# Performance work log

Hardware: AMD Instinct MI355X
Metric: run time of the kernel (lower is better)

The kernel has to match this reference:

```python
import jax, jax.numpy as jnp
import numpy as np

CH = 256
DQK = CH // 8

def setup_inputs() -> dict:
    key = jax.random.key(0)
    ks = jax.random.split(key, 8)
    x = jax.random.normal(ks[0], (4, 64, 64, CH), dtype=jnp.float32)
    # 1x1 convs == per-position linear layers: weight [Cin, Cout], bias [Cout]
    Wq = jax.random.normal(ks[1], (CH, DQK), dtype=jnp.float32) * 0.05
    bq = jnp.zeros((DQK,), dtype=jnp.float32)
    Wk = jax.random.normal(ks[2], (CH, DQK), dtype=jnp.float32) * 0.05
    bk = jnp.zeros((DQK,), dtype=jnp.float32)
    Wv = jax.random.normal(ks[3], (CH, CH), dtype=jnp.float32) * 0.05
    bv = jnp.zeros((CH,), dtype=jnp.float32)
    gamma = jnp.asarray(0.5, dtype=jnp.float32)  # nonzero so attention path matters
    return {"x": x, "Wq": Wq, "bq": bq, "Wk": Wk, "bk": bk, "Wv": Wv, "bv": bv, "gamma": gamma}

def reference(x, Wq, bq, Wk, bk, Wv, bv, gamma):
    B, H, W, C = x.shape
    N = H * W
    xf = x.reshape(B, N, C)                      # flatten spatial positions
    q = xf @ Wq + bq                             # [B, N, C/8]
    k = xf @ Wk + bk                             # [B, N, C/8]
    v = xf @ Wv + bv                             # [B, N, C]
    # Note: original applies NO 1/sqrt(d) scaling
    scores = jnp.einsum('bnd,bmd->bnm', q, k)    # [B, N, N]
    attn = jax.nn.softmax(scores, axis=-1)
    out = jnp.einsum('bnm,bmc->bnc', attn, v)    # [B, N, C]
    out = out.reshape(B, H, W, C)
    return gamma * out + x
```

## Files before the change

kernel.cpp:

```cpp
#include <hip/hip_runtime.h>


using short8 = __attribute__((ext_vector_type(8))) short;
using f32x4  = __attribute__((ext_vector_type(4))) float;
using f32x16 = __attribute__((ext_vector_type(16))) float;
using int4v  = __attribute__((ext_vector_type(4))) int;
using us4    = __attribute__((ext_vector_type(4))) unsigned short;

#define MFMA16(a,b,c) __builtin_amdgcn_mfma_f32_16x16x32_bf16((a),(b),(c),0,0,0)
#define MFMA32(a,b,c) __builtin_amdgcn_mfma_f32_32x32x16_bf16((a),(b),(c),0,0,0)

__device__ __forceinline__ unsigned short f2bf(float f) {
  union { float f; unsigned int u; } a; a.f = f;
  unsigned int u = a.u;
  return (unsigned short)((u + 0x7fffu + ((u >> 16) & 1u)) >> 16);
}
__device__ __forceinline__ float bf2f(unsigned short h) {
  union { unsigned int u; float f; } a; a.u = ((unsigned int)h) << 16;
  return a.f;
}
__device__ __forceinline__ unsigned int cvtpk(float lo, float hi) {
  unsigned int r;
  asm("v_cvt_pk_bf16_f32 %0, %1, %2" : "=v"(r) : "v"(lo), "v"(hi));
  return r;
}
__device__ __forceinline__ float xhalf_max(float v) {
  return fmaxf(v, __shfl_xor(v, 32));
}
__device__ __forceinline__ float xhalf_add(float v) {
  return v + __shfl_xor(v, 32);
}

__global__ __launch_bounds__(64) void pack_w_kernel(
    const float* __restrict__ Wq, const float* __restrict__ bq,
    const float* __restrict__ Wk, const float* __restrict__ bk,
    const float* __restrict__ Wv, const float* __restrict__ bv,
    unsigned short* __restrict__ Wf, unsigned short* __restrict__ Wlo,
    float* __restrict__ bcat)
{
  const int c = blockIdx.x;
  const int t = threadIdx.x;
  const float* W; int cc, stride;
  if (c < 32)      { W = Wq; cc = c;      stride = 32;  }
  else if (c < 64) { W = Wk; cc = c - 32; stride = 32;  }
  else             { W = Wv; cc = c - 64; stride = 256; }
  const int ct = c >> 4, lr = c & 15;
  for (int k = t; k < 256; k += 64) {
    float w = W[(size_t)k * stride + cc];
    unsigned short hi = f2bf(w);
    const int ks = k >> 5, lg = (k >> 3) & 3, j = k & 7;
    const int idx = (((ct * 8 + ks) * 64) + lr + 16 * lg) * 8 + j;
    Wf[idx] = hi;
    if (c < 64) Wlo[idx] = f2bf(w - bf2f(hi));
  }
  if (t == 0)
    bcat[c] = (c < 32) ? bq[c] : (c < 64) ? bk[c - 32] : bv[c - 64];
}

__global__ __launch_bounds__(256, 4) void qkv_kernel(
    const float* __restrict__ x,
    const unsigned short* __restrict__ Wf,
    const unsigned short* __restrict__ Wlo,
    const float* __restrict__ bcat,
    unsigned short* __restrict__ Qb, unsigned short* __restrict__ Kf,
    unsigned short* __restrict__ Vf)
{
  const int tid = threadIdx.x, wid = tid >> 6;
  const int l = tid & 63, lr = l & 15, lg = l >> 4;
  const int row0 = blockIdx.x * 16;

  short8 ahi[8], alo[8];
  const float* xr = x + (size_t)(row0 + lr) * 256 + lg * 8;
  #pragma unroll
  for (int ks = 0; ks < 8; ++ks) {
    f32x4 v0 = *(const f32x4*)(xr + ks * 32);
    f32x4 v1 = *(const f32x4*)(xr + ks * 32 + 4);
    short8 h, lo2;
    #pragma unroll
    for (int j = 0; j < 4; ++j) {
      unsigned short h0 = f2bf(v0[j]), h1 = f2bf(v1[j]);
      h[j] = (short)h0; h[j + 4] = (short)h1;
      lo2[j]     = (short)f2bf(v0[j] - bf2f(h0));
      lo2[j + 4] = (short)f2bf(v1[j] - bf2f(h1));
    }
    ahi[ks] = h; alo[ks] = lo2;
  }

  const int bb = row0 >> 12;
  const int n0loc = row0 & 4095;
  #pragma unroll
  for (int i = 0; i < 5; ++i) {
    const int ct = wid + i * 4;
    f32x4 acc = (f32x4){0.f, 0.f, 0.f, 0.f};
    const unsigned short* wbase = Wf + (size_t)(ct * 8) * 512 + l * 8;
    #pragma unroll
    for (int ks = 0; ks < 8; ++ks) {
      short8 bh = *(const short8*)(wbase + ks * 512);
      acc = MFMA16(ahi[ks], bh, acc);
    }
    if (i == 0) {
      const unsigned short* lbase = Wlo + (size_t)(ct * 8) * 512 + l * 8;
      #pragma unroll
      for (int ks = 0; ks < 8; ++ks) {
        short8 bh = *(const short8*)(wbase + ks * 512);
        short8 bl = *(const short8*)(lbase + ks * 512);
        acc = MFMA16(alo[ks], bh, acc);
        acc = MFMA16(ahi[ks], bl, acc);
      }
    }
    const int col = ct * 16 + lr;
    const float bias = bcat[col];
    unsigned short h[4];
    #pragma unroll
    for (int r = 0; r < 4; ++r) h[r] = f2bf(acc[r] + bias);

    if (col < 32) {
      #pragma unroll
      for (int r = 0; r < 4; ++r) {
        const int row = lg * 4 + r;
        Qb[(size_t)(row0 + row) * 32 + col] = h[r];
      }
    } else if (col < 64) {
      const int d = col - 32, dh = d >> 3, j = d & 7;
      const int kvb = n0loc >> 5, lq0 = (n0loc & 16);
      #pragma unroll
      for (int r = 0; r < 4; ++r) {
        const int lq = lq0 + lg * 4 + r;
        Kf[(size_t)(((bb * 128 + kvb) * 128) + lq + 32 * dh) * 8 + j] = h[r];
      }
    } else {
      const int cv = col - 64, ctv = cv >> 5, lc = cv & 31;
      const int kb = n0loc >> 4, kh = lg >> 1, j0 = 4 * (lg & 1);
      us4 pk = (us4){h[0], h[1], h[2], h[3]};
      *(us4*)(Vf + (size_t)((((bb * 8 + ctv) * 256 + kb) * 64) + lc + 32 * kh) * 8 + j0) = pk;
    }
  }
}

__global__ __launch_bounds__(256, 3) void attn_kernel(
    const unsigned short* __restrict__ Qb,
    const unsigned short* __restrict__ Kf,
    const unsigned short* __restrict__ Vf,
    const float* __restrict__ x,
    const float* __restrict__ gamma_p,
    float* __restrict__ out)
{
  const int tid = threadIdx.x, wid = tid >> 6;
  const int l = tid & 63, lq = l & 31, lh = l >> 5;

  const int bid = blockIdx.x;
  const int b  = (bid & 7) >> 1;
  const int u  = ((bid >> 3) << 1) | (bid & 1);
  const int qt = u >> 1, ch = u & 1;
  const int n0 = qt << 5;
  const int c0 = ch << 7;

  const unsigned short* qrow = Qb + (size_t)(b * 4096 + n0 + lq) * 32 + lh * 8;
  const short8 qf0 = *(const short8*)(qrow);
  const short8 qf1 = *(const short8*)(qrow + 16);

  f32x16 O[4];
  #pragma unroll
  for (int cc = 0; cc < 4; ++cc)
    #pragma unroll
    for (int r = 0; r < 16; ++r) O[cc][r] = 0.f;
  float m = -1e30f, lsum = 0.f;

  const int kv0 = wid << 10;
  for (int it = 0; it < 32; ++it) {
    const int kv = kv0 + (it << 5);

    const unsigned short* kp = Kf + (size_t)((b * 128 + (kv >> 5)) * 128) * 8 + l * 8;
    short8 kf0 = *(const short8*)(kp);
    short8 kf1 = *(const short8*)(kp + 512);
    f32x16 S;
    #pragma unroll
    for (int r = 0; r < 16; ++r) S[r] = 0.f;
    S = MFMA32(kf0, qf0, S);
    S = MFMA32(kf1, qf1, S);

    float mx = S[0];
    #pragma unroll
    for (int r = 1; r < 16; ++r) mx = fmaxf(mx, S[r]);
    mx = xhalf_max(mx);

    if (__any((int)(mx > m + 8.f))) {
      float mn = fmaxf(m, mx);
      float sc = __expf(m - mn);
      m = mn; lsum *= sc;
      #pragma unroll
      for (int cc = 0; cc < 4; ++cc)
        #pragma unroll
        for (int r = 0; r < 16; ++r) O[cc][r] *= sc;
    }

    float s = 0.f;
    #pragma unroll
    for (int r = 0; r < 16; ++r) { S[r] = __expf(S[r] - m); s += S[r]; }
    lsum += xhalf_add(s);

    unsigned int a0 = cvtpk(S[0], S[1]),  b0w = cvtpk(S[2], S[3]);
    unsigned int c0w = cvtpk(S[4], S[5]), d0w = cvtpk(S[6], S[7]);
    unsigned int pa0 = (unsigned int)__shfl_xor((int)a0, 32);
    unsigned int pb0 = (unsigned int)__shfl_xor((int)b0w, 32);
    unsigned int pc0 = (unsigned int)__shfl_xor((int)c0w, 32);
    unsigned int pd0 = (unsigned int)__shfl_xor((int)d0w, 32);
    int4v w0;
    w0[0] = (int)(lh ? pc0 : a0);
    w0[1] = (int)(lh ? pd0 : b0w);
    w0[2] = (int)(lh ? c0w : pa0);
    w0[3] = (int)(lh ? d0w : pb0);

    unsigned int a1 = cvtpk(S[8], S[9]),   b1w = cvtpk(S[10], S[11]);
    unsigned int c1w = cvtpk(S[12], S[13]), d1w = cvtpk(S[14], S[15]);
    unsigned int pa1 = (unsigned int)__shfl_xor((int)a1, 32);
    unsigned int pb1 = (unsigned int)__shfl_xor((int)b1w, 32);
    unsigned int pc1 = (unsigned int)__shfl_xor((int)c1w, 32);
    unsigned int pd1 = (unsigned int)__shfl_xor((int)d1w, 32);
    int4v w1;
    w1[0] = (int)(lh ? pc1 : a1);
    w1[1] = (int)(lh ? pd1 : b1w);
    w1[2] = (int)(lh ? c1w : pa1);
    w1[3] = (int)(lh ? d1w : pb1);

    short8 pb_0 = *(short8*)&w0;
    short8 pb_1 = *(short8*)&w1;

    const int kb = kv >> 4;
    #pragma unroll
    for (int cc = 0; cc < 4; ++cc) {
      const unsigned short* vp =
          Vf + (size_t)(((b * 8 + ch * 4 + cc) * 256 + kb) * 64) * 8 + l * 8;
      short8 vf0 = *(const short8*)(vp);
      short8 vf1 = *(const short8*)(vp + 512);
      O[cc] = MFMA32(vf0, pb_0, O[cc]);
      O[cc] = MFMA32(vf1, pb_1, O[cc]);
    }
  }

  __shared__ float msh[4][32];
  __shared__ float lsh[4][32];
  __shared__ float Osh[32][133];

  if (lh == 0) msh[wid][lq] = m;
  __syncthreads();
  const float M = fmaxf(fmaxf(msh[0][lq], msh[1][lq]),
                        fmaxf(msh[2][lq], msh[3][lq]));
  const float sw = __expf(m - M);
  lsum *= sw;
  if (lh == 0) lsh[wid][lq] = lsum;
  #pragma unroll
  for (int w = 0; w < 4; ++w) {
    __syncthreads();
    if (wid == w) {
      #pragma unroll
      for (int cc = 0; cc < 4; ++cc)
        #pragma unroll
        for (int r = 0; r < 16; ++r) {
          const int c = cc * 32 + (r & 3) + ((r >> 2) << 3) + (lh << 2);
          float v = sw * O[cc][r];
          float* p = &Osh[lq][c];
          if (w == 0) *p = v; else *p += v;
        }
    }
  }
  __syncthreads();

  const float g = gamma_p[0];
  #pragma unroll
  for (int i = 0; i < 4; ++i) {
    const int p = tid + (i << 8);
    const int q = p >> 5, c = (p & 31) << 2;
    const float L = lsh[0][q] + lsh[1][q] + lsh[2][q] + lsh[3][q];
    const float s = g / L;
    const size_t idx = (size_t)(b * 4096 + n0 + q) * 256 + c0 + c;
    f32x4 xi = *(const f32x4*)(x + idx);
    f32x4 res;
    #pragma unroll
    for (int j = 0; j < 4; ++j) res[j] = Osh[q][c + j] * s + xi[j];
    *(f32x4*)(out + idx) = res;
  }
}

extern "C" void kernel_launch(void* const* d_in, const int* in_sizes, int n_in,
                              void* d_out, int out_size, void* d_ws, size_t ws_size,
                              hipStream_t stream)
{
  const float* x     = (const float*)d_in[0];
  const float* Wq    = (const float*)d_in[1];
  const float* bq    = (const float*)d_in[2];
  const float* Wk    = (const float*)d_in[3];
  const float* bk    = (const float*)d_in[4];
  const float* Wv    = (const float*)d_in[5];
  const float* bv    = (const float*)d_in[6];
  const float* gamma = (const float*)d_in[7];
  float* out = (float*)d_out;

  char* ws = (char*)d_ws;
  unsigned short* Qb  = (unsigned short*)(ws);
  unsigned short* Kf  = (unsigned short*)(ws + (1u << 20));
  unsigned short* Vf  = (unsigned short*)(ws + (2u << 20));
  unsigned short* Wf  = (unsigned short*)(ws + (10u << 20));
  unsigned short* Wlo = (unsigned short*)(ws + (10u << 20) + (256u << 10));
  float*          bcat = (float*)(ws + (10u << 20) + (320u << 10));

  pack_w_kernel<<<dim3(320), dim3(64), 0, stream>>>(Wq, bq, Wk, bk, Wv, bv, Wf, Wlo, bcat);
  qkv_kernel<<<dim3(1024), dim3(256), 0, stream>>>(x, Wf, Wlo, bcat, Qb, Kf, Vf);
  attn_kernel<<<dim3(1024), dim3(256), 0, stream>>>(Qb, Kf, Vf, x, gamma, out);
}
```

Measured before the change: 177.5 us.

## Permute V layout to drop P cross-half shuffles; interleave QKV MFMA with x loads

The V fragment layout written by the QKV kernel is permuted (kh and j0 roles swapped) so the attention kernel can feed the exp'd score registers straight into the PV MFMA, without eight cross-half shuffles and selects per iteration. The QKV kernel now issues MFMAs for all five column tiles as each k-slice of x is converted, instead of keeping 16 short8 A fragments live. The row max uses a tree reduction. These cut shuffle latency in the attention inner loop and register pressure in the projection. Correctness depends on the new V layout matching the MFMA operand ordering exactly.

```diff
diff --git a/kernel.cpp b/kernel.cpp
--- a/kernel.cpp
+++ b/kernel.cpp
@@ -68,8 +68,13 @@
   const int tid = threadIdx.x, wid = tid >> 6;
   const int l = tid & 63, lr = l & 15, lg = l >> 4;
   const int row0 = blockIdx.x * 16;
-
-  short8 ahi[8], alo[8];
+  const int bb = row0 >> 12;
+  const int n0loc = row0 & 4095;
+
+  f32x4 acc[5];
+  #pragma unroll
+  for (int i = 0; i < 5; ++i) acc[i] = (f32x4){0.f, 0.f, 0.f, 0.f};
+
   const float* xr = x + (size_t)(row0 + lr) * 256 + lg * 8;
   #pragma unroll
   for (int ks = 0; ks < 8; ++ks) {
@@ -83,43 +88,32 @@
       lo2[j]     = (short)f2bf(v0[j] - bf2f(h0));
       lo2[j + 4] = (short)f2bf(v1[j] - bf2f(h1));
     }
-    ahi[ks] = h; alo[ks] = lo2;
-  }
-
-  const int bb = row0 >> 12;
-  const int n0loc = row0 & 4095;
+    #pragma unroll
+    for (int i = 0; i < 5; ++i) {
+      const int ct = wid + i * 4;
+      short8 bh = *(const short8*)(Wf + (size_t)((ct * 8 + ks) * 64 + l) * 8);
+      acc[i] = MFMA16(h, bh, acc[i]);
+      if (i == 0) {
+        short8 bl = *(const short8*)(Wlo + (size_t)((wid * 8 + ks) * 64 + l) * 8);
+        acc[0] = MFMA16(lo2, bh, acc[0]);
+        acc[0] = MFMA16(h, bl, acc[0]);
+      }
+    }
+  }
+
   #pragma unroll
   for (int i = 0; i < 5; ++i) {
     const int ct = wid + i * 4;
-    f32x4 acc = (f32x4){0.f, 0.f, 0.f, 0.f};
-    const unsigned short* wbase = Wf + (size_t)(ct * 8) * 512 + l * 8;
-    #pragma unroll
-    for (int ks = 0; ks < 8; ++ks) {
-      short8 bh = *(const short8*)(wbase + ks * 512);
-      acc = MFMA16(ahi[ks], bh, acc);
-    }
-    if (i == 0) {
-      const unsigned short* lbase = Wlo + (size_t)(ct * 8) * 512 + l * 8;
-      #pragma unroll
-      for (int ks = 0; ks < 8; ++ks) {
-        short8 bh = *(const short8*)(wbase + ks * 512);
-        short8 bl = *(const short8*)(lbase + ks * 512);
-        acc = MFMA16(alo[ks], bh, acc);
-        acc = MFMA16(ahi[ks], bl, acc);
-      }
-    }
     const int col = ct * 16 + lr;
     const float bias = bcat[col];
     unsigned short h[4];
     #pragma unroll
-    for (int r = 0; r < 4; ++r) h[r] = f2bf(acc[r] + bias);
+    for (int r = 0; r < 4; ++r) h[r] = f2bf(acc[i][r] + bias);
 
     if (col < 32) {
       #pragma unroll
-      for (int r = 0; r < 4; ++r) {
-        const int row = lg * 4 + r;
-        Qb[(size_t)(row0 + row) * 32 + col] = h[r];
-      }
+      for (int r = 0; r < 4; ++r)
+        Qb[(size_t)(row0 + lg * 4 + r) * 32 + col] = h[r];
     } else if (col < 64) {
       const int d = col - 32, dh = d >> 3, j = d & 7;
       const int kvb = n0loc >> 5, lq0 = (n0loc & 16);
@@ -130,7 +124,7 @@
       }
     } else {
       const int cv = col - 64, ctv = cv >> 5, lc = cv & 31;
-      const int kb = n0loc >> 4, kh = lg >> 1, j0 = 4 * (lg & 1);
+      const int kb = n0loc >> 4, kh = lg & 1, j0 = 4 * (lg >> 1);
       us4 pk = (us4){h[0], h[1], h[2], h[3]};
       *(us4*)(Vf + (size_t)((((bb * 8 + ctv) * 256 + kb) * 64) + lc + 32 * kh) * 8 + j0) = pk;
     }
@@ -179,10 +173,11 @@
     S = MFMA32(kf0, qf0, S);
     S = MFMA32(kf1, qf1, S);
 
-    float mx = S[0];
-    #pragma unroll
-    for (int r = 1; r < 16; ++r) mx = fmaxf(mx, S[r]);
-    mx = xhalf_max(mx);
+    float t0 = fmaxf(fmaxf(S[0], S[1]),  fmaxf(S[2], S[3]));
+    float t1 = fmaxf(fmaxf(S[4], S[5]),  fmaxf(S[6], S[7]));
+    float t2 = fmaxf(fmaxf(S[8], S[9]),  fmaxf(S[10], S[11]));
+    float t3 = fmaxf(fmaxf(S[12], S[13]), fmaxf(S[14], S[15]));
+    float mx = xhalf_max(fmaxf(fmaxf(t0, t1), fmaxf(t2, t3)));
 
     if (__any((int)(mx > m + 8.f))) {
       float mn = fmaxf(m, mx);
@@ -199,30 +194,11 @@
     for (int r = 0; r < 16; ++r) { S[r] = __expf(S[r] - m); s += S[r]; }
     lsum += xhalf_add(s);
 
-    unsigned int a0 = cvtpk(S[0], S[1]),  b0w = cvtpk(S[2], S[3]);
-    unsigned int c0w = cvtpk(S[4], S[5]), d0w = cvtpk(S[6], S[7]);
-    unsigned int pa0 = (unsigned int)__shfl_xor((int)a0, 32);
-    unsigned int pb0 = (unsigned int)__shfl_xor((int)b0w, 32);
-    unsigned int pc0 = (unsigned int)__shfl_xor((int)c0w, 32);
-    unsigned int pd0 = (unsigned int)__shfl_xor((int)d0w, 32);
-    int4v w0;
-    w0[0] = (int)(lh ? pc0 : a0);
-    w0[1] = (int)(lh ? pd0 : b0w);
-    w0[2] = (int)(lh ? c0w : pa0);
-    w0[3] = (int)(lh ? d0w : pb0);
-
-    unsigned int a1 = cvtpk(S[8], S[9]),   b1w = cvtpk(S[10], S[11]);
-    unsigned int c1w = cvtpk(S[12], S[13]), d1w = cvtpk(S[14], S[15]);
-    unsigned int pa1 = (unsigned int)__shfl_xor((int)a1, 32);
-    unsigned int pb1 = (unsigned int)__shfl_xor((int)b1w, 32);
-    unsigned int pc1 = (unsigned int)__shfl_xor((int)c1w, 32);
-    unsigned int pd1 = (unsigned int)__shfl_xor((int)d1w, 32);
-    int4v w1;
-    w1[0] = (int)(lh ? pc1 : a1);
-    w1[1] = (int)(lh ? pd1 : b1w);
-    w1[2] = (int)(lh ? c1w : pa1);
-    w1[3] = (int)(lh ? d1w : pb1);
-
+    int4v w0, w1;
+    w0[0] = (int)cvtpk(S[0], S[1]);   w0[1] = (int)cvtpk(S[2], S[3]);
+    w0[2] = (int)cvtpk(S[4], S[5]);   w0[3] = (int)cvtpk(S[6], S[7]);
+    w1[0] = (int)cvtpk(S[8], S[9]);   w1[1] = (int)cvtpk(S[10], S[11]);
+    w1[2] = (int)cvtpk(S[12], S[13]); w1[3] = (int)cvtpk(S[14], S[15]);
     short8 pb_0 = *(short8*)&w0;
     short8 pb_1 = *(short8*)&w1;
 
```

Result: faster. 166.0 us (-6.5%).
